# Optimization experiments

Measured on AMD Instinct MI355X. Metric: run time of the kernel, lower is better.

Reference implementation:

```python
import jax, jax.numpy as jnp
import numpy as np

B, T, D_MODEL = 2, 1024, 1024
HEAD_DIM = 128
NUM_HEADS = D_MODEL // HEAD_DIM          # 8
EXPAND_V = 1
HEAD_V = HEAD_DIM * EXPAND_V             # 128
KEY_DIM = NUM_HEADS * HEAD_DIM           # 1024
VALUE_DIM = NUM_HEADS * HEAD_V           # 1024
CONV_SIZE = 4
NUM_LEVELS = int(np.log2(T)) + 1         # 11 Fenwick levels
EPS = 1e-5
SCALE = HEAD_DIM ** -0.5


def setup_inputs() -> dict:
    ks = jax.random.split(jax.random.key(0), 20)
    w = lambda i, shp: 0.02 * jax.random.normal(ks[i], shp, jnp.float32)
    return {
        'x': jax.random.normal(ks[0], (B, T, D_MODEL), jnp.float32),
        'cos': jax.random.normal(ks[1], (T, HEAD_DIM), jnp.float32),
        'sin': jax.random.normal(ks[2], (T, HEAD_DIM), jnp.float32),
        'Wq': w(3, (D_MODEL, KEY_DIM)),
        'Wk': w(4, (D_MODEL, KEY_DIM)),
        'Wv': w(5, (D_MODEL, VALUE_DIM)),
        'Wb': w(6, (D_MODEL, NUM_HEADS)),
        'Wa': w(7, (D_MODEL, NUM_HEADS)),
        'Wl': w(8, (D_MODEL, NUM_HEADS * NUM_LEVELS)),
        'Wg': w(9, (D_MODEL, VALUE_DIM)),
        'Wo': w(10, (VALUE_DIM, D_MODEL)),
        'conv_q': 0.2 * jax.random.normal(ks[11], (KEY_DIM, CONV_SIZE), jnp.float32),
        'conv_k': 0.2 * jax.random.normal(ks[12], (KEY_DIM, CONV_SIZE), jnp.float32),
        'conv_v': 0.2 * jax.random.normal(ks[13], (VALUE_DIM, CONV_SIZE), jnp.float32),
        'A_log': jnp.log(jax.random.uniform(ks[14], (NUM_HEADS,), jnp.float32, 1.0, 16.0)),
        'dt_bias': jnp.log(jnp.expm1(jax.random.uniform(ks[15], (NUM_HEADS,), jnp.float32, 0.001, 0.1))),
        'norm_w': jnp.ones((HEAD_V,), jnp.float32),
    }


def _dwconv_silu(x, w):
    # causal depthwise conv1d (ShortConvolution, activation=silu). x:[B,T,C], w:[C,K]
    xp = jnp.pad(x, ((0, 0), (CONV_SIZE - 1, 0), (0, 0)))
    y = jax.lax.conv_general_dilated(xp, w.T[:, None, :], (1,), 'VALID',
                                     dimension_numbers=('NHC', 'HIO', 'NHC'),
                                     feature_group_count=w.shape[0])
    return jax.nn.silu(y)


def _l2norm(x):
    return x * jax.lax.rsqrt(jnp.sum(x * x, -1, keepdims=True) + 1e-6)


def _levels():
    # Fenwick-tree level of token s (0-indexed) in the prefix decomposition at time t:
    # level(t,s) = floor(log2((t+1) XOR s)) for s <= t.
    n = jnp.arange(1, T + 1, dtype=jnp.int32)[:, None]
    s = jnp.arange(T, dtype=jnp.int32)[None, :]
    xval = jnp.maximum(jnp.bitwise_xor(n, s), 1)
    lev = jnp.floor(jnp.log2(xval.astype(jnp.float32))).astype(jnp.int32)
    return jnp.clip(lev, 0, NUM_LEVELS - 1)  # [T,T]


def _forward(x, Wq, Wk, Wv, Wb, Wa, Wl, Wg, Wo, conv_q, conv_k, conv_v, A_log, dt_bias, norm_w):
    # projections + short conv + silu, split heads -> [B,H,T,d]
    q = _dwconv_silu(x @ Wq, conv_q).reshape(B, T, NUM_HEADS, HEAD_DIM).transpose(0, 2, 1, 3)
    k = _dwconv_silu(x @ Wk, conv_k).reshape(B, T, NUM_HEADS, HEAD_DIM).transpose(0, 2, 1, 3)
    v = _dwconv_silu(x @ Wv, conv_v).reshape(B, T, NUM_HEADS, HEAD_V).transpose(0, 2, 1, 3)
    q = _l2norm(q) * SCALE
    k = _l2norm(k)
    beta = jax.nn.sigmoid(x @ Wb).transpose(0, 2, 1)                      # [B,H,T]
    g = -jnp.exp(A_log) * jax.nn.softplus(x @ Wa + dt_bias)              # [B,T,H] log-decay per step
    gc = jnp.cumsum(g.transpose(0, 2, 1), axis=-1)                        # [B,H,T]
    lam = jax.nn.sigmoid(x @ Wl).reshape(B, T, NUM_HEADS, NUM_LEVELS).transpose(0, 2, 1, 3)  # [B,H,T,L]

    idx = jnp.arange(T)
    causal = idx[:, None] >= idx[None, :]
    strict = idx[:, None] > idx[None, :]
    # stable decay matrix D[t,s] = exp(gc_t - gc_s) <= 1 for s <= t
    logD = gc[..., :, None] - gc[..., None, :]
    Dm = jnp.exp(jnp.where(causal, logD, -jnp.inf))                       # [B,H,T,T]

    # WY / UT transform of the gated delta rule:
    #   u_t = beta_t * v_t - beta_t * sum_{s<t} (k_t . k_s) exp(gc_t-gc_s) u_s
    Akk = jnp.einsum('bhtd,bhsd->bhts', k, k) * Dm * strict
    u = jax.scipy.linalg.solve_triangular(beta[..., None] * Akk,
                                          beta[..., None] * v,
                                          lower=True, unit_diagonal=True)  # [B,H,T,dv]

    # log-linear (hierarchical) readout: o_t = sum_s lam_t[level(t,s)] * (q_t.k_s) D[t,s] * u_s
    P = jnp.einsum('bhtd,bhsd->bhts', q, k) * Dm
    M = jnp.take_along_axis(lam, _levels()[None, None], axis=3)           # [B,H,T,T]
    o = jnp.einsum('bhts,bhsd->bhtd', P * M, u).transpose(0, 2, 1, 3)      # [B,T,H,dv]

    # gated RMSNorm output gate, then output projection
    gate = (x @ Wg).reshape(B, T, NUM_HEADS, HEAD_V)
    o = o * jax.lax.rsqrt(jnp.mean(o * o, -1, keepdims=True) + EPS) * norm_w * jax.nn.silu(gate)
    return o.reshape(B, T, VALUE_DIM) @ Wo


def reference(x, cos, sin, Wq, Wk, Wv, Wb, Wa, Wl, Wg, Wo, conv_q, conv_k, conv_v, A_log, dt_bias, norm_w):
    # cos/sin are accepted (block signature) but unused, matching the source module.
    return _forward(x, Wq, Wk, Wv, Wb, Wa, Wl, Wg, Wo, conv_q, conv_k, conv_v, A_log, dt_bias, norm_w)
```

## Files before the change

kernel.cpp:

```cpp
#include <hip/hip_runtime.h>
#include <hip/hip_bf16.h>
#include <math.h>

#define SCALE_Q 0.08838834764831845f

typedef __bf16 bf16x8 __attribute__((ext_vector_type(8)));
typedef float f32x4 __attribute__((ext_vector_type(4)));

static __device__ __forceinline__ float sigm(float x){ return 1.f/(1.f+__expf(-x)); }
static __device__ __forceinline__ ushort f2b(float v){
  __hip_bfloat16 t = __float2bfloat16(v);
  return __builtin_bit_cast(ushort, t);
}
static __device__ __forceinline__ float b2f(ushort u){
  unsigned v = (unsigned)u << 16; return __builtin_bit_cast(float, v);
}

__global__ __launch_bounds__(256) void prep_all(const float* __restrict__ Wq,
    const float* __restrict__ Wk, const float* __restrict__ Wv,
    const float* __restrict__ Wg, const float* __restrict__ Wo,
    const float* __restrict__ X, const float* __restrict__ Wb,
    const float* __restrict__ Wa, const float* __restrict__ Wl,
    ushort* __restrict__ Wt4, ushort* __restrict__ Wot,
    ushort* __restrict__ x16, float* __restrict__ Wsm)
{
  int z = blockIdx.z;
  int tid = threadIdx.x;
  int flat = blockIdx.y * 32 + blockIdx.x;
  if (z < 5) {
    __shared__ float tile[32][36];
    const float* W = (z==0)?Wq:(z==1)?Wk:(z==2)?Wv:(z==3)?Wg:Wo;
    ushort* Wt = (z<4)? (Wt4 + (size_t)z*1048576) : Wot;
    int n0 = blockIdx.x*32, k0 = blockIdx.y*32;
    int r = tid >> 3, c4 = (tid & 7) << 2;
    *(float4*)&tile[r][c4] = *(const float4*)&W[(size_t)(k0 + r)*1024 + n0 + c4];
    __syncthreads();
    ushort4 o;
    o.x = f2b(tile[c4+0][r]); o.y = f2b(tile[c4+1][r]);
    o.z = f2b(tile[c4+2][r]); o.w = f2b(tile[c4+3][r]);
    *(ushort4*)&Wt[(size_t)(n0 + r)*1024 + k0 + c4] = o;
  } else if (z < 7) {
    int idx = (z-5)*262144 + flat*256 + tid;
    float4 v = *(const float4*)&X[(size_t)idx*4];
    ushort4 o; o.x=f2b(v.x); o.y=f2b(v.y); o.z=f2b(v.z); o.w=f2b(v.w);
    *(ushort4*)&x16[(size_t)idx*4] = o;
  } else {
    int idx = flat*256 + tid;
    if (idx < 1024*104) {
      int k = idx / 104, c = idx % 104;
      float v = (c < 8) ? Wb[k*8+c] : (c < 16) ? Wa[k*8+(c-8)] : Wl[k*88+(c-16)];
      Wsm[idx] = v;
    }
  }
}

__global__ __launch_bounds__(256) void gemm_bf16(const ushort* __restrict__ A,
    const ushort* __restrict__ Bt, void* __restrict__ C0, float* __restrict__ C1,
    int M, int N, int K, int nsplit, int ld0, int ld1, int c0bf16)
{
  __shared__ ushort As[3][128*32];
  __shared__ ushort Bs[3][128*32];
  int tid = threadIdx.x;
  int gx = gridDim.x;
  int nwg = gx * gridDim.y;
  int id = blockIdx.y * gx + blockIdx.x;
  int id2 = (id & 7) * (nwg >> 3) + (id >> 3);
  int bm = (id2 / gx) * 128, bn = (id2 % gx) * 128;
  int wave = tid >> 6, lane = tid & 63;
  int wm = (wave >> 1) * 64, wn = (wave & 1) * 64;
  int l16 = lane & 15, kh = lane >> 4;
  f32x4 acc[4][4] = {};
  int rowA0 = tid >> 2, boA = (tid & 3) * 16;
  int niter = K >> 5;

  #pragma unroll
  for (int s = 0; s < 2; ++s) {
    int k0 = s << 5;
    #pragma unroll
    for (int j = 0; j < 2; ++j) {
      int row = rowA0 + j*64;
      const char* gA = (const char*)A + (((size_t)(bm+row)*K + k0)*2 + boA);
      const char* gB = (const char*)Bt + (((size_t)(bn+row)*K + k0)*2 + boA);
      __builtin_amdgcn_global_load_lds((const __attribute__((address_space(1))) unsigned*)gA,
        (__attribute__((address_space(3))) unsigned*)((char*)&As[s][0] + row*64 + boA), 16, 0, 0);
      __builtin_amdgcn_global_load_lds((const __attribute__((address_space(1))) unsigned*)gB,
        (__attribute__((address_space(3))) unsigned*)((char*)&Bs[s][0] + row*64 + boA), 16, 0, 0);
    }
  }
  asm volatile("s_waitcnt vmcnt(4)" ::: "memory");
  __builtin_amdgcn_s_barrier();
  __builtin_amdgcn_sched_barrier(0);
  for (int i = 0; i < niter; ++i) {
    int cur = i % 3;
    if (i + 2 < niter) {
      int k0 = (i+2) << 5;
      int nb = (i+2) % 3;
      char* al = (char*)&As[nb][0];
      char* bl = (char*)&Bs[nb][0];
      #pragma unroll
      for (int j = 0; j < 2; ++j) {
        int row = rowA0 + j*64;
        const char* gA = (const char*)A + (((size_t)(bm+row)*K + k0)*2 + boA);
        const char* gB = (const char*)Bt + (((size_t)(bn+row)*K + k0)*2 + boA);
        __builtin_amdgcn_global_load_lds((const __attribute__((address_space(1))) unsigned*)gA,
          (__attribute__((address_space(3))) unsigned*)(al + row*64 + boA), 16, 0, 0);
        __builtin_amdgcn_global_load_lds((const __attribute__((address_space(1))) unsigned*)gB,
          (__attribute__((address_space(3))) unsigned*)(bl + row*64 + boA), 16, 0, 0);
      }
    }
    bf16x8 af[4], bfr[4];
    #pragma unroll
    for (int ii = 0; ii < 4; ++ii)
      af[ii] = *(bf16x8*)((char*)&As[cur][0] + (wm + ii*16 + l16)*64 + kh*16);
    #pragma unroll
    for (int j = 0; j < 4; ++j)
      bfr[j] = *(bf16x8*)((char*)&Bs[cur][0] + (wn + j*16 + l16)*64 + kh*16);
    #pragma unroll
    for (int ii = 0; ii < 4; ++ii)
      #pragma unroll
      for (int j = 0; j < 4; ++j)
        acc[ii][j] = __builtin_amdgcn_mfma_f32_16x16x32_bf16(af[ii], bfr[j], acc[ii][j], 0, 0, 0);
    if (i + 1 < niter) {
      if (i + 2 < niter) {
        asm volatile("s_waitcnt vmcnt(4) lgkmcnt(0)" ::: "memory");
      } else {
        asm volatile("s_waitcnt vmcnt(0) lgkmcnt(0)" ::: "memory");
      }
      __builtin_amdgcn_s_barrier();
      __builtin_amdgcn_sched_barrier(0);
    }
  }
  int rg = lane >> 4;
  #pragma unroll
  for (int i = 0; i < 4; ++i) {
    #pragma unroll
    for (int j = 0; j < 4; ++j) {
      int col = bn + wn + j*16 + l16;
      #pragma unroll
      for (int r = 0; r < 4; ++r) {
        int row = bm + wm + i*16 + rg*4 + r;
        float v = acc[i][j][r];
        if (col < nsplit) {
          if (c0bf16) ((ushort*)C0)[(size_t)row*ld0 + col] = f2b(v);
          else        ((float*)C0)[(size_t)row*ld0 + col] = v;
        } else C1[(size_t)row*ld1 + (col - nsplit)] = v;
      }
    }
  }
}

__global__ __launch_bounds__(256) void skinny104(const float* __restrict__ X,
    const float* __restrict__ Wsm, float* __restrict__ part)
{
  __shared__ float XL[64][132];
  __shared__ float WsL[128][112];
  int tid = threadIdx.x;
  int m0 = blockIdx.x << 6;
  int k0 = blockIdx.y << 7;
  #pragma unroll
  for (int j = 0; j < 8; ++j) {
    int s = tid + j*256;
    int row = s >> 5, c4 = (s & 31) << 2;
    *(float4*)&XL[row][c4] = *(const float4*)&X[(size_t)(m0 + row)*1024 + k0 + c4];
  }
  {
    int k = tid >> 1, c = 104 + ((tid & 1) << 2);
    *(float4*)&WsL[k][c] = (float4){0.f,0.f,0.f,0.f};
  }
  {
    int k = tid >> 1, cb = (tid & 1) * 52;
    #pragma unroll
    for (int j = 0; j < 13; ++j) {
      *(float4*)&WsL[k][cb + j*4] = *(const float4*)&Wsm[(size_t)(k0 + k)*104 + cb + j*4];
    }
  }
  __syncthreads();
  int row = tid >> 2, cq = tid & 3;
  int cbase = cq * 28;
  f32x4 acc[7] = {};
  const float* xrow = &XL[row][0];
  #pragma unroll 4
  for (int k = 0; k < 128; ++k) {
    float xv = xrow[k];
    const f32x4* wr = (const f32x4*)&WsL[k][cbase];
    #pragma unroll
    for (int j = 0; j < 7; ++j) acc[j] += xv * wr[j];
  }
  float* pr = &part[((size_t)blockIdx.y*2048 + m0 + row)*104 + cbase];
  int nst = (cq == 3) ? 5 : 7;
  for (int j = 0; j < nst; ++j) *(f32x4*)&pr[j*4] = acc[j];
}

__global__ __launch_bounds__(256) void reduce8(const float* __restrict__ part,
    float* __restrict__ xs)
{
  int idx = blockIdx.x*256 + threadIdx.x;
  if (idx >= 212992) return;
  float s = 0.f;
  #pragma unroll
  for (int i = 0; i < 8; ++i) s += part[(size_t)i*212992 + idx];
  xs[idx] = s;
}

__global__ __launch_bounds__(256) void conv_fused(const ushort* __restrict__ Xall,
    const float* __restrict__ Wq, const float* __restrict__ Wk, const float* __restrict__ Wv,
    ushort* __restrict__ qb16, ushort* __restrict__ kb16, ushort* __restrict__ vb16, int ldx)
{
  int mode = blockIdx.y;
  const float* W = (mode==0)?Wq:(mode==1)?Wk:Wv;
  const ushort* X = Xall + mode*1024;
  int row = blockIdx.x;
  int b = row >> 10, t = row & 1023;
  int tid = threadIdx.x;
  int c0 = tid << 2;
  float w[4][4];
  #pragma unroll
  for (int c = 0; c < 4; ++c) {
    float4 wv = *(const float4*)&W[(c0 + c)*4];
    w[c][0]=wv.x; w[c][1]=wv.y; w[c][2]=wv.z; w[c][3]=wv.w;
  }
  float acc[4] = {0.f,0.f,0.f,0.f};
  #pragma unroll
  for (int j = 0; j < 4; ++j) {
    int tt = t - 3 + j;
    if (tt >= 0) {
      ushort4 xv = *(const ushort4*)&X[(size_t)(b*1024 + tt)*ldx + c0];
      acc[0] += w[0][j]*b2f(xv.x); acc[1] += w[1][j]*b2f(xv.y);
      acc[2] += w[2][j]*b2f(xv.z); acc[3] += w[3][j]*b2f(xv.w);
    }
  }
  #pragma unroll
  for (int c = 0; c < 4; ++c) acc[c] *= sigm(acc[c]);
  if (mode < 2) {
    float ss = acc[0]*acc[0]+acc[1]*acc[1]+acc[2]*acc[2]+acc[3]*acc[3];
    ss += __shfl_xor(ss, 1); ss += __shfl_xor(ss, 2); ss += __shfl_xor(ss, 4);
    ss += __shfl_xor(ss, 8); ss += __shfl_xor(ss, 16);
    float r = rsqrtf(ss + 1e-6f);
    if (mode == 0) r *= SCALE_Q;
    acc[0]*=r; acc[1]*=r; acc[2]*=r; acc[3]*=r;
  }
  size_t o = (size_t)(b*1024 + t)*1024 + c0;
  ushort* Y = (mode==0)?qb16:(mode==1)?kb16:vb16;
  ushort4 yb; yb.x=f2b(acc[0]); yb.y=f2b(acc[1]); yb.z=f2b(acc[2]); yb.w=f2b(acc[3]);
  *(ushort4*)&Y[o] = yb;
}

__global__ __launch_bounds__(256) void gc2(const float* __restrict__ xs,
    const float* __restrict__ A_log, const float* __restrict__ dt_bias,
    float* __restrict__ gc)
{
  int bh = blockIdx.x, b = bh >> 3, h = bh & 7;
  __shared__ float sc[256];
  int tid = threadIdx.x;
  float aexp = __expf(A_log[h]), db = dt_bias[h];
  int t0 = tid*4;
  float g[4], csum = 0.f;
  #pragma unroll
  for (int z = 0; z < 4; ++z) {
    float zv = xs[(size_t)(b*1024 + t0 + z)*104 + 8 + h] + db;
    float sp = (zv > 20.f) ? zv : log1pf(__expf(zv));
    csum += -aexp*sp;
    g[z] = csum;
  }
  sc[tid] = csum;
  __syncthreads();
  for (int ofs = 1; ofs < 256; ofs <<= 1) {
    float v = (tid >= ofs) ? sc[tid-ofs] : 0.f;
    __syncthreads();
    sc[tid] += v;
    __syncthreads();
  }
  float excl = sc[tid] - csum;
  #pragma unroll
  for (int z = 0; z < 4; ++z) gc[bh*1024 + t0 + z] = excl + g[z];
}

__global__ __launch_bounds__(256) void chunk_prep(const ushort* __restrict__ Kg16,
    const ushort* __restrict__ Vg16, const float* __restrict__ xs,
    const float* __restrict__ gcg, float* __restrict__ cw, ushort* __restrict__ cWk16,
    ushort* __restrict__ cKpT16, float* __restrict__ eD)
{
  int blk = blockIdx.x;
  int bh = blk >> 4, ck = blk & 15;
  int b = bh >> 3, h = bh & 7;
  int a = ck << 6;
  __shared__ ushort Kl[64*128];
  __shared__ float As[64][68];
  __shared__ float gcl[65];
  __shared__ float bl[64];
  __shared__ float egc[64];
  __shared__ float edt[64];
  int tid = threadIdx.x;
  int wave = tid >> 6, lane = tid & 63;
  int l15 = lane & 15, kh = lane >> 4;
  for (int e = tid; e < 2048; e += 256) {
    int t = e >> 5;
    int c4u = (e & 31) << 2;
    ushort4 kv = *(const ushort4*)&Kg16[(size_t)(b*1024 + a + t)*1024 + h*128 + c4u];
    unsigned slot = (unsigned)(c4u >> 3) ^ (unsigned)(t & 15);
    *(ushort4*)((char*)Kl + t*256 + slot*16 + (c4u & 7)*2) = kv;
  }
  if (tid < 64) {
    gcl[tid] = gcg[bh*1024 + a + tid];
    bl[tid] = sigm(xs[(size_t)(b*1024 + a + tid)*104 + h]);
  }
  if (tid == 64) gcl[64] = (ck < 15) ? gcg[bh*1024 + a + 64] : 0.f;
  __syncthreads();
  if (tid < 64) {
    egc[tid] = __expf(gcl[tid] - gcl[0]);
    edt[tid] = (ck < 15) ? __expf(gcl[64] - gcl[tid]) : 0.f;
  }
  {
    int arow = wave*16 + l15;
    int asw = arow & 15;
    for (int jt = 0; jt <= wave; ++jt) {
      int brow = jt*16 + l15;
      int bsw = brow & 15;
      f32x4 acc = {0.f,0.f,0.f,0.f};
      #pragma unroll
      for (int ks = 0; ks < 4; ++ks) {
        bf16x8 afr = *(const bf16x8*)((char*)Kl + arow*256 + (((ks*4 + kh) ^ asw) << 4));
        bf16x8 bfr = *(const bf16x8*)((char*)Kl + brow*256 + (((ks*4 + kh) ^ bsw) << 4));
        acc = __builtin_amdgcn_mfma_f32_16x16x32_bf16(afr, bfr, acc, 0, 0, 0);
      }
      int s = jt*16 + l15;
      #pragma unroll
      for (int r = 0; r < 4; ++r) {
        int t = wave*16 + kh*4 + r;
        if (s < t) As[t][s] = bl[t]*acc[r]*__expf(gcl[t]-gcl[s]);
      }
    }
  }
  __syncthreads();
  int c = tid;
  float u[64];
  if (c < 128) {
    #pragma unroll
    for (int t = 0; t < 64; ++t)
      u[t] = bl[t]*b2f(Vg16[(size_t)(b*1024 + a + t)*1024 + h*128 + c]);
  } else {
    int d = c - 128;
    unsigned dslot = (unsigned)(d >> 3);
    #pragma unroll
    for (int t = 0; t < 64; ++t) {
      ushort kv = *(const ushort*)((char*)Kl + t*256 + ((dslot ^ (unsigned)(t & 15)) << 4) + (d & 7)*2);
      u[t] = bl[t]*egc[t]*b2f(kv);
    }
  }
  #pragma unroll
  for (int t = 1; t < 64; ++t) {
    float acc = u[t];
    int s = 0;
    #pragma unroll
    for (; s + 4 <= t; s += 4) {
      float4 a4 = *(float4*)&As[t][s];
      acc -= a4.x*u[s] + a4.y*u[s+1] + a4.z*u[s+2] + a4.w*u[s+3];
    }
    #pragma unroll
    for (; s < t; ++s) acc -= As[t][s]*u[s];
    u[t] = acc;
  }
  size_t cbase = (size_t)blk*8192;
  if (c < 128) {
    #pragma unroll
    for (int t = 0; t < 64; ++t)
      cw[cbase + t*128 + c] = u[t];
  } else {
    int d = c - 128;
    unsigned dslot = (unsigned)(d >> 3);
    #pragma unroll
    for (int t = 0; t < 64; ++t) {
      cWk16[cbase + t*128 + d] = f2b(-u[t]);
      ushort kv = *(const ushort*)((char*)Kl + t*256 + ((dslot ^ (unsigned)(t & 15)) << 4) + (d & 7)*2);
      cKpT16[cbase + d*64 + t] = f2b(b2f(kv)*edt[t]);
    }
  }
  if (tid == 0) eD[blk] = (ck < 15) ? __expf(gcl[64]-gcl[0]) : 0.f;
}

__global__ __launch_bounds__(256) void chunk_scan6(const float* __restrict__ cw,
    const ushort* __restrict__ cWk16, const ushort* __restrict__ cKpT16,
    const float* __restrict__ eD, ushort* __restrict__ Ut)
{
  int blk = blockIdx.x;
  int slice = blk >> 4, bh = blk & 15;
  int e_base = slice << 3;
  __shared__ ushort Wks[2][8192];
  __shared__ ushort Kps[2][8192];
  __shared__ ushort StT[16*128];
  __shared__ ushort usT[16*64];
  __shared__ float  Stf[128*16];
  int tid = threadIdx.x;
  int wave = tid >> 6, lane = tid & 63;
  int l15 = lane & 15, kh = lane >> 4;
  for (int idx = tid; idx < 16*128; idx += 256) StT[idx] = 0;
  for (int idx = tid; idx < 16*64; idx += 256) usT[idx] = 0;
  for (int idx = tid; idx < 128*16; idx += 256) Stf[idx] = 0.f;

  int e = l15;
  int t0 = wave*16 + kh*4;
  int ci0 = bh << 4;
  f32x4 wcur = {0.f,0.f,0.f,0.f};
  if (e < 8) {
    #pragma unroll
    for (int r = 0; r < 4; ++r)
      wcur[r] = cw[(size_t)ci0*8192 + (t0+r)*128 + e_base + e];
  }
  {
    const char* wg = (const char*)(cWk16 + (size_t)ci0*8192);
    const char* kg = (const char*)(cKpT16 + (size_t)ci0*8192);
    #pragma unroll
    for (int j = 0; j < 4; ++j) {
      unsigned off = (j<<12) + (tid<<4);
      unsigned wrow = off >> 8, wslot = (off >> 4) & 15;
      unsigned wsrc = wrow*256 + ((wslot ^ (wrow & 15)) << 4);
      __builtin_amdgcn_global_load_lds((const __attribute__((address_space(1))) unsigned*)(wg + wsrc),
        (__attribute__((address_space(3))) unsigned*)((char*)&Wks[0][0] + off), 16, 0, 0);
      unsigned krow = off >> 7, kslot = (off >> 4) & 7;
      unsigned ksrc = krow*128 + ((kslot ^ (krow & 7)) << 4);
      __builtin_amdgcn_global_load_lds((const __attribute__((address_space(1))) unsigned*)(kg + ksrc),
        (__attribute__((address_space(3))) unsigned*)((char*)&Kps[0][0] + off), 16, 0, 0);
    }
  }
  __syncthreads();

  for (int i = 0; i < 16; ++i) {
    int ci = ci0 + i, a = i << 6, cur = i & 1;
    f32x4 wnext = {0.f,0.f,0.f,0.f};
    if (i < 15) {
      if (e < 8) {
        #pragma unroll
        for (int r = 0; r < 4; ++r)
          wnext[r] = cw[(size_t)(ci+1)*8192 + (t0+r)*128 + e_base + e];
      }
      const char* wg = (const char*)(cWk16 + (size_t)(ci+1)*8192);
      const char* kg = (const char*)(cKpT16 + (size_t)(ci+1)*8192);
      char* wl = (char*)&Wks[cur^1][0];
      char* kl = (char*)&Kps[cur^1][0];
      #pragma unroll
      for (int j = 0; j < 4; ++j) {
        unsigned off = (j<<12) + (tid<<4);
        unsigned wrow = off >> 8, wslot = (off >> 4) & 15;
        unsigned wsrc = wrow*256 + ((wslot ^ (wrow & 15)) << 4);
        __builtin_amdgcn_global_load_lds((const __attribute__((address_space(1))) unsigned*)(wg + wsrc),
          (__attribute__((address_space(3))) unsigned*)(wl + off), 16, 0, 0);
        unsigned krow = off >> 7, kslot = (off >> 4) & 7;
        unsigned ksrc = krow*128 + ((kslot ^ (krow & 7)) << 4);
        __builtin_amdgcn_global_load_lds((const __attribute__((address_space(1))) unsigned*)(kg + ksrc),
          (__attribute__((address_space(3))) unsigned*)(kl + off), 16, 0, 0);
      }
    }
    {
      f32x4 d = wcur;
      const char* wkb = (const char*)&Wks[cur][0];
      int arow = wave*16 + l15;
      #pragma unroll
      for (int ks = 0; ks < 4; ++ks) {
        bf16x8 afr = *(const bf16x8*)(wkb + arow*256 + (((ks*4 + kh) ^ l15) << 4));
        bf16x8 bfr = *(const bf16x8*)((const char*)StT + l15*256 + (((ks*4 + kh) ^ l15) << 4));
        d = __builtin_amdgcn_mfma_f32_16x16x32_bf16(afr, bfr, d, 0, 0, 0);
      }
      if (e < 8) {
        ushort4 uw;
        uw.x = f2b(d[0]); uw.y = f2b(d[1]); uw.z = f2b(d[2]); uw.w = f2b(d[3]);
        *(ushort4*)((char*)usT + e*128 + (((t0>>3) ^ (e&7)) << 4) + (t0&7)*2) = uw;
        *(ushort4*)&Ut[(size_t)(bh*128 + e_base + e)*1024 + a + t0] = uw;
      }
    }
    asm volatile("s_waitcnt lgkmcnt(0)" ::: "memory");
    __builtin_amdgcn_s_barrier();
    __builtin_amdgcn_sched_barrier(0);
    if (i < 15) {
      float ed = eD[ci];
      const char* kpb = (const char*)&Kps[cur][0];
      #pragma unroll
      for (int mt = 0; mt < 2; ++mt) {
        int krow = (wave*2 + mt)*16 + l15;
        int k0 = (wave*2 + mt)*16 + kh*4;
        f32x4 c;
        #pragma unroll
        for (int r = 0; r < 4; ++r) c[r] = ed * Stf[(k0+r)*16 + e];
        #pragma unroll
        for (int ts = 0; ts < 2; ++ts) {
          bf16x8 afr = *(const bf16x8*)(kpb + krow*128 + (((ts*4 + kh) ^ (krow&7)) << 4));
          bf16x8 bfr = *(const bf16x8*)((const char*)usT + l15*128 + (((ts*4 + kh) ^ (l15&7)) << 4));
          c = __builtin_amdgcn_mfma_f32_16x16x32_bf16(afr, bfr, c, 0, 0, 0);
        }
        #pragma unroll
        for (int r = 0; r < 4; ++r) Stf[(k0+r)*16 + e] = c[r];
        if (e < 8) {
          ushort4 sw;
          sw.x = f2b(c[0]); sw.y = f2b(c[1]); sw.z = f2b(c[2]); sw.w = f2b(c[3]);
          *(ushort4*)((char*)StT + e*256 + (((k0>>3) ^ e) << 4) + (k0&7)*2) = sw;
        }
      }
      wcur = wnext;
      asm volatile("s_waitcnt vmcnt(0) lgkmcnt(0)" ::: "memory");
      __builtin_amdgcn_s_barrier();
      __builtin_amdgcn_sched_barrier(0);
    }
  }
}

__global__ __launch_bounds__(256) void readout3(const ushort* __restrict__ Qb,
    const ushort* __restrict__ Kb, const ushort* __restrict__ Ut,
    const float* __restrict__ gcg, const float* __restrict__ xs,
    float* __restrict__ Og)
{
  int blk = blockIdx.x;
  int bh = blk >> 4, ic = blk & 15;
  int half = blockIdx.y;
  int b = bh >> 3, h = bh & 7;
  int tbase = ic << 6;
  __shared__ ushort Ks[2][8192];
  __shared__ ushort Us[2][8192];
  __shared__ ushort Pl[4][1024];
  __shared__ float lamS[64][12];
  int tid = threadIdx.x;
  int wave = tid >> 6, lane = tid & 63;
  int l15 = lane & 15, kh = lane >> 4;

  const char* kgb = (const char*)Kb + ((size_t)(b*1024)*1024 + h*128)*2;
  const char* ugb = (const char*)Ut + ((size_t)(bh*128)*1024)*2;

  for (int e = tid; e < 64*11; e += 256) {
    int t = e/11, l = e%11;
    lamS[t][l] = sigm(xs[(size_t)(b*1024+tbase+t)*104 + 16 + h*11 + l]);
  }
  int tl = kh*4;
  float gct_r[4];
  #pragma unroll
  for (int r = 0; r < 4; ++r) gct_r[r] = gcg[bh*1024 + tbase + wave*16 + tl + r];
  bf16x8 qf[4];
  {
    const ushort* qp = &Qb[(size_t)(b*1024 + tbase + wave*16 + l15)*1024 + h*128 + kh*8];
    #pragma unroll
    for (int kk = 0; kk < 4; ++kk) qf[kk] = *(const bf16x8*)(qp + kk*32);
  }

  f32x4 accO[8] = {};
  int nsteps = ic + 1;
  int jmid = (nsteps + 1) >> 1;
  int j0 = half ? jmid : 0;
  int j1 = half ? nsteps : jmid;
  ushort* Pw = &Pl[wave][0];

  if (j0 < j1) {
    {
      const char* kg = kgb + (size_t)(j0<<6)*2048;
      const char* ug = ugb + (size_t)(j0<<6)*2;
      #pragma unroll
      for (int it = 0; it < 4; ++it) {
        unsigned off = (it<<12) + (tid<<4);
        unsigned krow = off >> 8, kc = (off >> 4) & 15;
        unsigned ksrc = krow*2048 + ((kc ^ (krow & 15)) << 4);
        __builtin_amdgcn_global_load_lds((const __attribute__((address_space(1))) unsigned*)(kg + ksrc),
          (__attribute__((address_space(3))) unsigned*)((char*)&Ks[0][0] + off), 16, 0, 0);
        unsigned ud = off >> 7, uc = (off >> 4) & 7;
        unsigned usrc = ud*2048 + ((uc ^ (ud & 7)) << 4);
        __builtin_amdgcn_global_load_lds((const __attribute__((address_space(1))) unsigned*)(ug + usrc),
          (__attribute__((address_space(3))) unsigned*)((char*)&Us[0][0] + off), 16, 0, 0);
      }
    }
    __syncthreads();
    int cur = 0;
    for (int j = j0; j < j1; ++j) {
      int sbase = j << 6;
      if (j + 1 < j1) {
        const char* kg = kgb + (size_t)((j+1)<<6)*2048;
        const char* ug = ugb + (size_t)((j+1)<<6)*2;
        char* kl = (char*)&Ks[cur^1][0];
        char* ul = (char*)&Us[cur^1][0];
        #pragma unroll
        for (int it = 0; it < 4; ++it) {
          unsigned off = (it<<12) + (tid<<4);
          unsigned krow = off >> 8, kc = (off >> 4) & 15;
          unsigned ksrc = krow*2048 + ((kc ^ (krow & 15)) << 4);
          __builtin_amdgcn_global_load_lds((const __attribute__((address_space(1))) unsigned*)(kg + ksrc),
            (__attribute__((address_space(3))) unsigned*)(kl + off), 16, 0, 0);
          unsigned ud = off >> 7, uc = (off >> 4) & 7;
          unsigned usrc = ud*2048 + ((uc ^ (ud & 7)) << 4);
          __builtin_amdgcn_global_load_lds((const __attribute__((address_space(1))) unsigned*)(ug + usrc),
            (__attribute__((address_space(3))) unsigned*)(ul + off), 16, 0, 0);
        }
      }
      float gcs_r[4];
      #pragma unroll
      for (int jt = 0; jt < 4; ++jt)
        gcs_r[jt] = gcg[bh*1024 + sbase + jt*16 + l15];
      f32x4 accS[4] = {};
      const char* ksb = (const char*)&Ks[cur][0];
      #pragma unroll
      for (int jt = 0; jt < 4; ++jt) {
        int row = jt*16 + l15;
        int rsw = row & 15;
        #pragma unroll
        for (int kk = 0; kk < 4; ++kk) {
          bf16x8 kf = *(const bf16x8*)(ksb + row*256 + (((kk*4 + kh) ^ rsw) << 4));
          accS[jt] = __builtin_amdgcn_mfma_f32_16x16x32_bf16(qf[kk], kf, accS[jt], 0, 0, 0);
        }
      }
      #pragma unroll
      for (int jt = 0; jt < 4; ++jt) {
        int sg = sbase + jt*16 + l15;
        #pragma unroll
        for (int r = 0; r < 4; ++r) {
          int t_loc = tl + r;
          int tg = tbase + wave*16 + t_loc;
          float pv = 0.f;
          if (sg <= tg) {
            int lev = 31 - __clz((unsigned)((tg+1) ^ sg));
            lev = lev > 10 ? 10 : lev;
            pv = accS[jt][r] * __expf(gct_r[r] - gcs_r[jt]) * lamS[wave*16 + t_loc][lev];
          }
          int bo = (t_loc << 7) + ((jt*16 + l15) << 1);
          bo ^= (t_loc & 7) << 4;
          *(ushort*)((char*)Pw + bo) = f2b(pv);
        }
      }
      const char* usb = (const char*)&Us[cur][0];
      #pragma unroll
      for (int ks = 0; ks < 2; ++ks) {
        int bo = (l15 << 7) + ((ks*32 + kh*8) << 1);
        bo ^= (l15 & 7) << 4;
        bf16x8 pa = *(bf16x8*)((char*)Pw + bo);
        #pragma unroll
        for (int dt = 0; dt < 8; ++dt) {
          int d = dt*16 + l15;
          bf16x8 uf = *(const bf16x8*)(usb + d*128 + (((ks*4 + kh) ^ (d & 7)) << 4));
          accO[dt] = __builtin_amdgcn_mfma_f32_16x16x32_bf16(pa, uf, accO[dt], 0, 0, 0);
        }
      }
      __syncthreads();
      cur ^= 1;
    }
  }
  float* og = Og + (size_t)half*2097152;
  #pragma unroll
  for (int dt = 0; dt < 8; ++dt) {
    #pragma unroll
    for (int r = 0; r < 4; ++r) {
      int row = tbase + wave*16 + tl + r;
      og[(size_t)(b*1024 + row)*1024 + h*128 + dt*16 + l15] = accO[dt][r];
    }
  }
}

__global__ __launch_bounds__(64) void normgate(const float* __restrict__ O1,
    const float* __restrict__ O2, const float* __restrict__ G,
    const float* __restrict__ norm_w, ushort* __restrict__ Y)
{
  int row = blockIdx.x;
  int lane = threadIdx.x;
  size_t base = (size_t)(row >> 3)*1024 + (size_t)(row & 7)*128;
  float2 oa = *(const float2*)&O1[base + lane*2];
  float2 ob = *(const float2*)&O2[base + lane*2];
  float ox = oa.x + ob.x, oy = oa.y + ob.y;
  float ss = ox*ox + oy*oy;
  #pragma unroll
  for (int m = 1; m < 64; m <<= 1) ss += __shfl_xor(ss, m);
  float r = rsqrtf(ss * (1.f/128.f) + 1e-5f);
  float2 g = *(const float2*)&G[base + lane*2];
  ushort2 y;
  y.x = f2b(ox * r * norm_w[lane*2+0] * (g.x * sigm(g.x)));
  y.y = f2b(oy * r * norm_w[lane*2+1] * (g.y * sigm(g.y)));
  *(ushort2*)&Y[base + lane*2] = y;
}

extern "C" void kernel_launch(void* const* d_in, const int* in_sizes, int n_in,
                              void* d_out, int out_size, void* d_ws, size_t ws_size,
                              hipStream_t stream)
{
  const float* x    = (const float*)d_in[0];
  const float* Wq   = (const float*)d_in[3];
  const float* Wk   = (const float*)d_in[4];
  const float* Wv   = (const float*)d_in[5];
  const float* Wb   = (const float*)d_in[6];
  const float* Wa   = (const float*)d_in[7];
  const float* Wl   = (const float*)d_in[8];
  const float* Wg   = (const float*)d_in[9];
  const float* Wo   = (const float*)d_in[10];
  const float* cq   = (const float*)d_in[11];
  const float* ck   = (const float*)d_in[12];
  const float* cv   = (const float*)d_in[13];
  const float* A_log   = (const float*)d_in[14];
  const float* dt_bias = (const float*)d_in[15];
  const float* norm_w  = (const float*)d_in[16];
  float* out = (float*)d_out;

  float* p = (float*)d_ws;
  float* xqkv = p;  p += 6291456;
  float* xg   = p;  p += 2097152;
  float* kbu  = p;  p += 2097152;
  float* vbu  = p;  p += 2097152;
  float* o1   = p;  p += 2097152;
  float* o2   = p;  p += 2097152;
  float* xs   = p;  p += 212992;
  float* gc   = p;  p += 16384;
  float* eD   = p;  p += 256;
  ushort* x16 = (ushort*)p; p += 1048576;
  ushort* Wt4 = (ushort*)p; p += 2097152;
  ushort* Wot = (ushort*)p; p += 524288;
  float* Wsm  = p;  p += 106496;
  ushort* yb16= (ushort*)p; p += 1048576;
  ushort* qb16= (ushort*)p; p += 1048576;
  ushort* kb16= (ushort*)p; p += 1048576;
  ushort* ut16= (ushort*)p; p += 1048576;
  ushort* xqkv16 = (ushort*)xqkv;
  ushort* vb16 = (ushort*)vbu;
  float* cw  = xqkv;
  ushort* cWk16  = (ushort*)(xqkv + 2097152);
  ushort* cKpT16 = (ushort*)(xqkv + 3145728);
  float* part = o1;
  (void)kbu;

  dim3 blk(256);
  prep_all<<<dim3(32,32,8), blk, 0, stream>>>(Wq, Wk, Wv, Wg, Wo, x, Wb, Wa, Wl,
                                              Wt4, Wot, x16, Wsm);
  gemm_bf16<<<dim3(32,16), blk, 0, stream>>>(x16, Wt4, xqkv16, xg, 2048, 4096, 1024,
                                             3072, 3072, 1024, 1);
  skinny104<<<dim3(32,8), blk, 0, stream>>>(x, Wsm, part);
  reduce8<<<dim3(833), blk, 0, stream>>>(part, xs);
  conv_fused<<<dim3(2048,3), blk, 0, stream>>>(xqkv16, cq, ck, cv, qb16, kb16, vb16, 3072);
  gc2<<<dim3(16), blk, 0, stream>>>(xs, A_log, dt_bias, gc);
  chunk_prep<<<dim3(256), blk, 0, stream>>>(kb16, vb16, xs, gc, cw, cWk16, cKpT16, eD);
  chunk_scan6<<<dim3(256), blk, 0, stream>>>(cw, cWk16, cKpT16, eD, ut16);
  readout3<<<dim3(256,2), blk, 0, stream>>>(qb16, kb16, ut16, gc, xs, o1);
  normgate<<<dim3(16384), dim3(64), 0, stream>>>(o1, o2, xg, norm_w, yb16);
  gemm_bf16<<<dim3(8,16), blk, 0, stream>>>(yb16, Wot, out, out, 2048, 1024, 1024,
                                            1024, 1024, 1024, 0);
}
```

Baseline: 193.0 us.

## Store gate in bf16, batch normgate rows, use 64-row tiles for Wo GEMM

The first GEMM now writes the gate projection (xg) as bf16 instead of fp32, which halves its write traffic and the read traffic in normgate. normgate now processes four rows per 256-thread block instead of one row per 64-thread block, cutting the block count. The output projection switches to a new 64x128-tile kernel with two waves, doubling the grid from 128 to 256 workgroups so more CUs are busy on the 2048x1024 GEMM. Rounding the gate to bf16 adds a small precision loss.

```diff
diff --git a/kernel.cpp b/kernel.cpp
--- a/kernel.cpp
+++ b/kernel.cpp
@@ -55,8 +55,8 @@
 }
 
 __global__ __launch_bounds__(256) void gemm_bf16(const ushort* __restrict__ A,
-    const ushort* __restrict__ Bt, void* __restrict__ C0, float* __restrict__ C1,
-    int M, int N, int K, int nsplit, int ld0, int ld1, int c0bf16)
+    const ushort* __restrict__ Bt, void* __restrict__ C0, void* __restrict__ C1,
+    int M, int N, int K, int nsplit, int ld0, int ld1, int c0bf16, int c1bf16)
 {
   __shared__ ushort As[3][128*32];
   __shared__ ushort Bs[3][128*32];
@@ -143,7 +143,108 @@
         if (col < nsplit) {
           if (c0bf16) ((ushort*)C0)[(size_t)row*ld0 + col] = f2b(v);
           else        ((float*)C0)[(size_t)row*ld0 + col] = v;
-        } else C1[(size_t)row*ld1 + (col - nsplit)] = v;
+        } else {
+          if (c1bf16) ((ushort*)C1)[(size_t)row*ld1 + (col - nsplit)] = f2b(v);
+          else        ((float*)C1)[(size_t)row*ld1 + (col - nsplit)] = v;
+        }
+      }
+    }
+  }
+}
+
+__global__ __launch_bounds__(128) void gemm_wo64(const ushort* __restrict__ A,
+    const ushort* __restrict__ Bt, float* __restrict__ C, int K)
+{
+  __shared__ ushort As[3][64*32];
+  __shared__ ushort Bs[3][128*32];
+  int tid = threadIdx.x;
+  int gx = gridDim.x;
+  int nwg = gx * gridDim.y;
+  int id = blockIdx.y * gx + blockIdx.x;
+  int id2 = (id & 7) * (nwg >> 3) + (id >> 3);
+  int bm = (id2 / gx) * 64, bn = (id2 % gx) * 128;
+  int wave = tid >> 6, lane = tid & 63;
+  int wn = wave * 64;
+  int l16 = lane & 15, kh = lane >> 4;
+  f32x4 acc[4][4] = {};
+  int rowA0 = tid >> 2, boA = (tid & 3) * 16;
+  int niter = K >> 5;
+
+  #pragma unroll
+  for (int s = 0; s < 2; ++s) {
+    int k0 = s << 5;
+    #pragma unroll
+    for (int j = 0; j < 2; ++j) {
+      int row = rowA0 + j*32;
+      const char* gA = (const char*)A + (((size_t)(bm+row)*K + k0)*2 + boA);
+      __builtin_amdgcn_global_load_lds((const __attribute__((address_space(1))) unsigned*)gA,
+        (__attribute__((address_space(3))) unsigned*)((char*)&As[s][0] + row*64 + boA), 16, 0, 0);
+    }
+    #pragma unroll
+    for (int j = 0; j < 4; ++j) {
+      int row = rowA0 + j*32;
+      const char* gB = (const char*)Bt + (((size_t)(bn+row)*K + k0)*2 + boA);
+      __builtin_amdgcn_global_load_lds((const __attribute__((address_space(1))) unsigned*)gB,
+        (__attribute__((address_space(3))) unsigned*)((char*)&Bs[s][0] + row*64 + boA), 16, 0, 0);
+    }
+  }
+  asm volatile("s_waitcnt vmcnt(6)" ::: "memory");
+  __builtin_amdgcn_s_barrier();
+  __builtin_amdgcn_sched_barrier(0);
+  for (int i = 0; i < niter; ++i) {
+    int cur = i % 3;
+    if (i + 2 < niter) {
+      int k0 = (i+2) << 5;
+      int nb = (i+2) % 3;
+      char* al = (char*)&As[nb][0];
+      char* bl = (char*)&Bs[nb][0];
+      #pragma unroll
+      for (int j = 0; j < 2; ++j) {
+        int row = rowA0 + j*32;
+        const char* gA = (const char*)A + (((size_t)(bm+row)*K + k0)*2 + boA);
+        __builtin_amdgcn_global_load_lds((const __attribute__((address_space(1))) unsigned*)gA,
+          (__attribute__((address_space(3))) unsigned*)(al + row*64 + boA), 16, 0, 0);
+      }
+      #pragma unroll
+      for (int j = 0; j < 4; ++j) {
+        int row = rowA0 + j*32;
+        const char* gB = (const char*)Bt + (((size_t)(bn+row)*K + k0)*2 + boA);
+        __builtin_amdgcn_global_load_lds((const __attribute__((address_space(1))) unsigned*)(gB),
+          (__attribute__((address_space(3))) unsigned*)(bl + row*64 + boA), 16, 0, 0);
+      }
+    }
+    bf16x8 af[4], bfr[4];
+    #pragma unroll
+    for (int ii = 0; ii < 4; ++ii)
+      af[ii] = *(bf16x8*)((char*)&As[cur][0] + (ii*16 + l16)*64 + kh*16);
+    #pragma unroll
+    for (int j = 0; j < 4; ++j)
+      bfr[j] = *(bf16x8*)((char*)&Bs[cur][0] + (wn + j*16 + l16)*64 + kh*16);
+    #pragma unroll
+    for (int ii = 0; ii < 4; ++ii)
+      #pragma unroll
+      for (int j = 0; j < 4; ++j)
+        acc[ii][j] = __builtin_amdgcn_mfma_f32_16x16x32_bf16(af[ii], bfr[j], acc[ii][j], 0, 0, 0);
+    if (i + 1 < niter) {
+      if (i + 2 < niter) {
+        asm volatile("s_waitcnt vmcnt(6) lgkmcnt(0)" ::: "memory");
+      } else {
+        asm volatile("s_waitcnt vmcnt(0) lgkmcnt(0)" ::: "memory");
+      }
+      __builtin_amdgcn_s_barrier();
+      __builtin_amdgcn_sched_barrier(0);
+    }
+  }
+  int rg = lane >> 4;
+  #pragma unroll
+  for (int i = 0; i < 4; ++i) {
+    #pragma unroll
+    for (int j = 0; j < 4; ++j) {
+      int col = bn + wn + j*16 + l16;
+      #pragma unroll
+      for (int r = 0; r < 4; ++r) {
+        int row = bm + i*16 + rg*4 + r;
+        C[(size_t)row*1024 + col] = acc[i][j][r];
       }
     }
   }
@@ -646,12 +747,12 @@
   }
 }
 
-__global__ __launch_bounds__(64) void normgate(const float* __restrict__ O1,
-    const float* __restrict__ O2, const float* __restrict__ G,
+__global__ __launch_bounds__(256) void normgate(const float* __restrict__ O1,
+    const float* __restrict__ O2, const ushort* __restrict__ G16,
     const float* __restrict__ norm_w, ushort* __restrict__ Y)
 {
-  int row = blockIdx.x;
-  int lane = threadIdx.x;
+  int row = blockIdx.x*4 + (threadIdx.x >> 6);
+  int lane = threadIdx.x & 63;
   size_t base = (size_t)(row >> 3)*1024 + (size_t)(row & 7)*128;
   float2 oa = *(const float2*)&O1[base + lane*2];
   float2 ob = *(const float2*)&O2[base + lane*2];
@@ -660,10 +761,11 @@
   #pragma unroll
   for (int m = 1; m < 64; m <<= 1) ss += __shfl_xor(ss, m);
   float r = rsqrtf(ss * (1.f/128.f) + 1e-5f);
-  float2 g = *(const float2*)&G[base + lane*2];
+  ushort2 g16 = *(const ushort2*)&G16[base + lane*2];
+  float gx = b2f(g16.x), gy = b2f(g16.y);
   ushort2 y;
-  y.x = f2b(ox * r * norm_w[lane*2+0] * (g.x * sigm(g.x)));
-  y.y = f2b(oy * r * norm_w[lane*2+1] * (g.y * sigm(g.y)));
+  y.x = f2b(ox * r * norm_w[lane*2+0] * (gx * sigm(gx)));
+  y.y = f2b(oy * r * norm_w[lane*2+1] * (gy * sigm(gy)));
   *(ushort2*)&Y[base + lane*2] = y;
 }
 
@@ -707,6 +809,7 @@
   ushort* kb16= (ushort*)p; p += 1048576;
   ushort* ut16= (ushort*)p; p += 1048576;
   ushort* xqkv16 = (ushort*)xqkv;
+  ushort* xg16 = (ushort*)xg;
   ushort* vb16 = (ushort*)vbu;
   float* cw  = xqkv;
   ushort* cWk16  = (ushort*)(xqkv + 2097152);
@@ -717,8 +820,8 @@
   dim3 blk(256);
   prep_all<<<dim3(32,32,8), blk, 0, stream>>>(Wq, Wk, Wv, Wg, Wo, x, Wb, Wa, Wl,
                                               Wt4, Wot, x16, Wsm);
-  gemm_bf16<<<dim3(32,16), blk, 0, stream>>>(x16, Wt4, xqkv16, xg, 2048, 4096, 1024,
-                                             3072, 3072, 1024, 1);
+  gemm_bf16<<<dim3(32,16), blk, 0, stream>>>(x16, Wt4, xqkv16, xg16, 2048, 4096, 1024,
+                                             3072, 3072, 1024, 1, 1);
   skinny104<<<dim3(32,8), blk, 0, stream>>>(x, Wsm, part);
   reduce8<<<dim3(833), blk, 0, stream>>>(part, xs);
   conv_fused<<<dim3(2048,3), blk, 0, stream>>>(xqkv16, cq, ck, cv, qb16, kb16, vb16, 3072);
@@ -726,7 +829,6 @@
   chunk_prep<<<dim3(256), blk, 0, stream>>>(kb16, vb16, xs, gc, cw, cWk16, cKpT16, eD);
   chunk_scan6<<<dim3(256), blk, 0, stream>>>(cw, cWk16, cKpT16, eD, ut16);
   readout3<<<dim3(256,2), blk, 0, stream>>>(qb16, kb16, ut16, gc, xs, o1);
-  normgate<<<dim3(16384), dim3(64), 0, stream>>>(o1, o2, xg, norm_w, yb16);
-  gemm_bf16<<<dim3(8,16), blk, 0, stream>>>(yb16, Wot, out, out, 2048, 1024, 1024,
-                                            1024, 1024, 1024, 0);
-}
+  normgate<<<dim3(4096), blk, 0, stream>>>(o1, o2, xg16, norm_w, yb16);
+  gemm_wo64<<<dim3(8,32), dim3(128), 0, stream>>>(yb16, Wot, out, 1024);
+}
```

Measured after the change: 189.7 us, median of 2. Within noise of the previous version (-1.7%).
